# Optimization experiments

Hardware: AMD Instinct MI355X
Metric: run time of the kernel (lower is better)

The kernel has to match this reference:

```python
import jax, jax.numpy as jnp
import numpy as np

EMBED_CHOICES = (512, 768, 1024)
RATIO_CHOICES = (2, 3, 4)
D_MAX = 1024           # max embed_dim
H_MAX = 4096           # max expansion dim = 1024 * 4


def setup_inputs() -> dict:
    key = jax.random.key(0)
    ks = jax.random.split(key, 7)
    return {
        "x": jax.random.normal(ks[0], (8, 512, D_MAX), dtype=jnp.float32),
        "w0": jax.random.normal(ks[1], (H_MAX, D_MAX), dtype=jnp.float32) * 0.02,
        "b0": jax.random.normal(ks[2], (H_MAX,), dtype=jnp.float32) * 0.02,
        "w1": jax.random.normal(ks[3], (D_MAX, H_MAX), dtype=jnp.float32) * 0.02,
        "b1": jax.random.normal(ks[4], (D_MAX,), dtype=jnp.float32) * 0.02,
        "arch_embed": jax.random.normal(ks[5], (3,), dtype=jnp.float32),
        "arch_mlp": jax.random.normal(ks[6], (3,), dtype=jnp.float32),
    }


def _effective_masks(a, b):
    """Weighted-sum-of-sliced-linears == single linear with masked effective weights.

    Candidate (e, r): uses W0[:e*r, :e] on x[..., :e], zero-padded to H_MAX,
    and W1[:e, :e*r] on h[..., :e*r], zero-padded to D_MAX.
    """
    col = jnp.arange(D_MAX)
    row = jnp.arange(H_MAX)
    m0 = jnp.zeros((H_MAX, D_MAX), dtype=jnp.float32)
    bm0 = jnp.zeros((H_MAX,), dtype=jnp.float32)
    m1 = jnp.zeros((D_MAX, H_MAX), dtype=jnp.float32)
    bm1 = jnp.zeros((D_MAX,), dtype=jnp.float32)
    for ie, e in enumerate(EMBED_CHOICES):
        cm = (col < e).astype(jnp.float32)          # [D_MAX]
        for ir, r in enumerate(RATIO_CHOICES):
            w = a[ie] * b[ir]
            rm = (row < e * r).astype(jnp.float32)  # [H_MAX]
            m0 = m0 + w * rm[:, None] * cm[None, :]
            bm0 = bm0 + w * rm
            m1 = m1 + w * cm[:, None] * rm[None, :]
            bm1 = bm1 + w * cm
    return m0, bm0, m1, bm1


def reference(x, w0, b0, w1, b1, arch_embed, arch_mlp):
    a = jax.nn.softmax(arch_embed)  # DARTS-style arch weights over embed_dim
    b = jax.nn.softmax(arch_mlp)    # over mlp_ratio
    m0, bm0, m1, bm1 = _effective_masks(a, b)
    # layer 0 mix: [B,S,D] @ [D,H] -> [B,S,H]
    h = jnp.einsum("bsd,hd->bsh", x, m0 * w0) + bm0 * b0
    h = jax.nn.relu(h)
    # layer 1 mix: [B,S,H] @ [H,D] -> [B,S,D]
    out = jnp.einsum("bsh,dh->bsd", h, m1 * w1) + bm1 * b1
    # dropout p=0.0 (eval): identity
    return out
```

## Files before the change

### kernel.cpp

```cpp
#include <hip/hip_runtime.h>


typedef __attribute__((ext_vector_type(8))) short bf16x8;
typedef __attribute__((ext_vector_type(4))) float f32x4;
typedef __attribute__((ext_vector_type(8))) unsigned short u16x8;

__device__ __forceinline__ unsigned short f2bf(float f) {
  unsigned int x = __float_as_uint(f);
  x += 0x7fffu + ((x >> 16) & 1u);
  return (unsigned short)(x >> 16);
}

__device__ __forceinline__ void softmax3(const float* __restrict__ p, float* o) {
  float m = fmaxf(p[0], fmaxf(p[1], p[2]));
  float e0 = expf(p[0] - m), e1 = expf(p[1] - m), e2 = expf(p[2] - m);
  float inv = 1.0f / (e0 + e1 + e2);
  o[0] = e0 * inv; o[1] = e1 * inv; o[2] = e2 * inv;
}

__device__ __forceinline__ float sval(int h, int d, const float a[3], const float b[3]) {
  constexpr int E[3] = {512, 768, 1024};
  constexpr int R[3] = {2, 3, 4};
  float s = 0.f;
#pragma unroll
  for (int ie = 0; ie < 3; ++ie) {
    if (d < E[ie]) {
      float t = 0.f;
#pragma unroll
      for (int ir = 0; ir < 3; ++ir)
        if (h < E[ie] * R[ir]) t += b[ir];
      s += a[ie] * t;
    }
  }
  return s;
}


__global__ __launch_bounds__(256) void conv_x(const float* __restrict__ x,
                                              unsigned short* __restrict__ o,
                                              int n8) {
  int t = blockIdx.x * 256 + threadIdx.x;
  if (t >= n8) return;
  const f32x4* p = (const f32x4*)(x + (size_t)t * 8);
  f32x4 v0 = p[0], v1 = p[1];
  u16x8 r;
#pragma unroll
  for (int j = 0; j < 4; ++j) { r[j] = f2bf(v0[j]); r[4 + j] = f2bf(v1[j]); }
  *(u16x8*)(o + (size_t)t * 8) = r;
}

__global__ __launch_bounds__(256) void conv_w0(const float* __restrict__ w,
                                               const float* __restrict__ ae,
                                               const float* __restrict__ am,
                                               unsigned short* __restrict__ o) {
  int t = blockIdx.x * 256 + threadIdx.x;
  int base = t * 8;
  int h = base >> 10, d = base & 1023;
  float a[3], b[3];
  softmax3(ae, a); softmax3(am, b);
  float s = sval(h, d, a, b);
  const f32x4* p = (const f32x4*)(w + (size_t)base);
  f32x4 v0 = p[0], v1 = p[1];
  u16x8 r;
#pragma unroll
  for (int j = 0; j < 4; ++j) { r[j] = f2bf(v0[j] * s); r[4 + j] = f2bf(v1[j] * s); }
  *(u16x8*)(o + (size_t)base) = r;
}

__global__ __launch_bounds__(256) void conv_w1(const float* __restrict__ w,
                                               const float* __restrict__ ae,
                                               const float* __restrict__ am,
                                               unsigned short* __restrict__ o) {
  int t = blockIdx.x * 256 + threadIdx.x;
  int base = t * 8;
  int d = base >> 12, h = base & 4095;
  float a[3], b[3];
  softmax3(ae, a); softmax3(am, b);
  float s = sval(h, d, a, b);
  const f32x4* p = (const f32x4*)(w + (size_t)base);
  f32x4 v0 = p[0], v1 = p[1];
  u16x8 r;
#pragma unroll
  for (int j = 0; j < 4; ++j) { r[j] = f2bf(v0[j] * s); r[4 + j] = f2bf(v1[j] * s); }
  *(u16x8*)(o + (size_t)base) = r;
}

__global__ __launch_bounds__(256) void conv_bias(const float* __restrict__ b0,
                                                 const float* __restrict__ b1,
                                                 const float* __restrict__ ae,
                                                 const float* __restrict__ am,
                                                 float* __restrict__ bb0,
                                                 float* __restrict__ bb1) {
  int i = blockIdx.x * 256 + threadIdx.x;
  float a[3], b[3];
  softmax3(ae, a); softmax3(am, b);
  if (i < 4096) bb0[i] = sval(i, 0, a, b) * b0[i];
  int d = i - 4096;
  if (d >= 0 && d < 1024) bb1[d] = sval(0, d, a, b) * b1[d];
}


template <int MODE>
__device__ __forceinline__ void gemm_core(const unsigned short* __restrict__ A,
                                          const unsigned short* __restrict__ B,
                                          const float* __restrict__ bias,
                                          void* __restrict__ Cout,
                                          int M, int N, int K, int Ksub) {
  __shared__ unsigned short As[128 * 64];
  __shared__ unsigned short Bs[128 * 64];

  const int tid  = threadIdx.x;
  const int lane = tid & 63;
  const int w    = tid >> 6;
  const int m0   = blockIdx.x * 128;
  const int n0   = blockIdx.y * 128;
  const int wm   = (w >> 1) * 64;
  const int wn   = (w & 1) * 64;
  const int kbeg = (MODE == 2) ? blockIdx.z * Ksub : 0;
  const int kend = kbeg + Ksub;

  f32x4 acc[4][4] = {};

  const int srow = tid >> 3;
  const int scol = (tid & 7) * 8;
  const unsigned short* Ag = A + (size_t)(m0 + srow) * K + scol;
  const unsigned short* Bg = B + (size_t)(n0 + srow) * K + scol;
  unsigned short* Asl = As + tid * 8;
  unsigned short* Bsl = Bs + tid * 8;

  for (int k0 = kbeg; k0 < kend; k0 += 64) {
    __syncthreads();
#pragma unroll
    for (int i = 0; i < 4; ++i) {
      __builtin_amdgcn_global_load_lds(
          (const __attribute__((address_space(1))) void*)(Ag + (size_t)(i * 32) * K + k0),
          (__attribute__((address_space(3))) void*)(Asl + i * 2048), 16, 0, 0);
      __builtin_amdgcn_global_load_lds(
          (const __attribute__((address_space(1))) void*)(Bg + (size_t)(i * 32) * K + k0),
          (__attribute__((address_space(3))) void*)(Bsl + i * 2048), 16, 0, 0);
    }
    asm volatile("s_waitcnt vmcnt(0)" ::: "memory");
    __syncthreads();

#pragma unroll
    for (int ks = 0; ks < 2; ++ks) {
      const int ko = ks * 32 + (lane >> 4) * 8;
      bf16x8 af[4], bfr[4];
#pragma unroll
      for (int m = 0; m < 4; ++m)
        af[m] = *(const bf16x8*)&As[(wm + m * 16 + (lane & 15)) * 64 + ko];
#pragma unroll
      for (int n = 0; n < 4; ++n)
        bfr[n] = *(const bf16x8*)&Bs[(wn + n * 16 + (lane & 15)) * 64 + ko];
#pragma unroll
      for (int m = 0; m < 4; ++m)
#pragma unroll
        for (int n = 0; n < 4; ++n)
          acc[m][n] = __builtin_amdgcn_mfma_f32_16x16x32_bf16(af[m], bfr[n], acc[m][n], 0, 0, 0);
    }
  }

  const int crow = (lane >> 4) * 4;
  const int ccol = lane & 15;
#pragma unroll
  for (int m = 0; m < 4; ++m) {
#pragma unroll
    for (int n = 0; n < 4; ++n) {
      const int gr = m0 + wm + m * 16 + crow;
      const int gc = n0 + wn + n * 16 + ccol;
      if (MODE == 0) {
        const float bv = bias[gc];
        unsigned short* H = (unsigned short*)Cout;
#pragma unroll
        for (int r = 0; r < 4; ++r) {
          float v = fmaxf(acc[m][n][r] + bv, 0.f);
          H[(size_t)(gr + r) * N + gc] = f2bf(v);
        }
      } else if (MODE == 1) {
        const float bv = bias[gc];
        float* C = (float*)Cout;
#pragma unroll
        for (int r = 0; r < 4; ++r)
          C[(size_t)(gr + r) * N + gc] = acc[m][n][r] + bv;
      } else {
        float* P = (float*)Cout + (size_t)blockIdx.z * M * N;
#pragma unroll
        for (int r = 0; r < 4; ++r)
          P[(size_t)(gr + r) * N + gc] = acc[m][n][r];
      }
    }
  }
}

__global__ __launch_bounds__(256) void gemm_h(const unsigned short* __restrict__ A,
                                              const unsigned short* __restrict__ B,
                                              const float* __restrict__ bias,
                                              void* __restrict__ C,
                                              int M, int N, int K, int Ksub) {
  gemm_core<0>(A, B, bias, C, M, N, K, Ksub);
}
__global__ __launch_bounds__(256) void gemm_f(const unsigned short* __restrict__ A,
                                              const unsigned short* __restrict__ B,
                                              const float* __restrict__ bias,
                                              void* __restrict__ C,
                                              int M, int N, int K, int Ksub) {
  gemm_core<1>(A, B, bias, C, M, N, K, Ksub);
}
__global__ __launch_bounds__(256) void gemm_p(const unsigned short* __restrict__ A,
                                              const unsigned short* __restrict__ B,
                                              const float* __restrict__ bias,
                                              void* __restrict__ C,
                                              int M, int N, int K, int Ksub) {
  gemm_core<2>(A, B, bias, C, M, N, K, Ksub);
}

__global__ __launch_bounds__(256) void reduce_k(const float* __restrict__ P,
                                                const float* __restrict__ bb1,
                                                float* __restrict__ out,
                                                int n4) {
  const f32x4* p = (const f32x4*)P;
  const f32x4* bv = (const f32x4*)bb1;
  f32x4* o = (f32x4*)out;
  for (int i = blockIdx.x * 256 + threadIdx.x; i < n4; i += gridDim.x * 256) {
    f32x4 v = p[i];
    v += p[i + n4];
    v += p[i + 2 * n4];
    v += p[i + 3 * n4];
    v += bv[i & 255];
    o[i] = v;
  }
}


extern "C" void kernel_launch(void* const* d_in, const int* in_sizes, int n_in,
                              void* d_out, int out_size, void* d_ws, size_t ws_size,
                              hipStream_t stream) {
  const float* x  = (const float*)d_in[0];
  const float* w0 = (const float*)d_in[1];
  const float* b0 = (const float*)d_in[2];
  const float* w1 = (const float*)d_in[3];
  const float* b1 = (const float*)d_in[4];
  const float* ae = (const float*)d_in[5];
  const float* am = (const float*)d_in[6];

  char* ws = (char*)d_ws;
  unsigned short* xb   = (unsigned short*)(ws);
  unsigned short* w0e  = (unsigned short*)(ws + (8u  << 20));
  unsigned short* w1e  = (unsigned short*)(ws + (16u << 20));
  unsigned short* Hbuf = (unsigned short*)(ws + (24u << 20));
  float* bb0 = (float*)(ws + (56u << 20));
  float* bb1 = (float*)(ws + (56u << 20) + 16384);
  float* part = (float*)(ws + (57u << 20));
  const size_t WS_NEEDED = (57u << 20) + (64u << 20);

  conv_x  <<<2048, 256, 0, stream>>>(x, xb, 524288);
  conv_w0 <<<2048, 256, 0, stream>>>(w0, ae, am, w0e);
  conv_w1 <<<2048, 256, 0, stream>>>(w1, ae, am, w1e);
  conv_bias<<<20, 256, 0, stream>>>(b0, b1, ae, am, bb0, bb1);

  dim3 g1(32, 32);
  gemm_h<<<g1, 256, 0, stream>>>(xb, w0e, bb0, Hbuf, 4096, 4096, 1024, 1024);

  if (ws_size >= WS_NEEDED) {
    dim3 g2(32, 8, 4);
    gemm_p<<<g2, 256, 0, stream>>>(Hbuf, w1e, nullptr, part, 4096, 1024, 4096, 1024);
    reduce_k<<<2048, 256, 0, stream>>>(part, bb1, (float*)d_out, 1024 * 1024);
  } else {
    dim3 g2(32, 8);
    gemm_f<<<g2, 256, 0, stream>>>(Hbuf, w1e, bb1, d_out, 4096, 1024, 4096, 4096);
  }
}
```

Measured before the change: 223.6 us.

## Double-buffer GEMM LDS tiles and fuse conversion kernels into one launch

The GEMM main loop now uses two LDS buffers and issues global-to-LDS loads for the next K tile before computing the current one, waiting only on the older loads. This is meant to overlap memory latency with MFMA work. The four fp32-to-bf16 conversion and bias kernels are also merged into a single launch to cut launch overhead. Doubling LDS to 64KB per block may lower occupancy.

```diff
diff --git a/kernel.cpp b/kernel.cpp
--- a/kernel.cpp
+++ b/kernel.cpp
@@ -36,67 +36,49 @@
 }
 
 
-__global__ __launch_bounds__(256) void conv_x(const float* __restrict__ x,
-                                              unsigned short* __restrict__ o,
-                                              int n8) {
-  int t = blockIdx.x * 256 + threadIdx.x;
-  if (t >= n8) return;
-  const f32x4* p = (const f32x4*)(x + (size_t)t * 8);
+__device__ __forceinline__ void cvt8(const float* __restrict__ src,
+                                     unsigned short* __restrict__ dst,
+                                     size_t base, float s) {
+  const f32x4* p = (const f32x4*)(src + base);
   f32x4 v0 = p[0], v1 = p[1];
   u16x8 r;
 #pragma unroll
-  for (int j = 0; j < 4; ++j) { r[j] = f2bf(v0[j]); r[4 + j] = f2bf(v1[j]); }
-  *(u16x8*)(o + (size_t)t * 8) = r;
-}
-
-__global__ __launch_bounds__(256) void conv_w0(const float* __restrict__ w,
-                                               const float* __restrict__ ae,
-                                               const float* __restrict__ am,
-                                               unsigned short* __restrict__ o) {
+  for (int j = 0; j < 4; ++j) { r[j] = f2bf(v0[j] * s); r[4 + j] = f2bf(v1[j] * s); }
+  *(u16x8*)(dst + base) = r;
+}
+
+__global__ __launch_bounds__(256) void conv_all(const float* __restrict__ x,
+                                                const float* __restrict__ w0,
+                                                const float* __restrict__ b0,
+                                                const float* __restrict__ w1,
+                                                const float* __restrict__ b1,
+                                                const float* __restrict__ ae,
+                                                const float* __restrict__ am,
+                                                unsigned short* __restrict__ xb,
+                                                unsigned short* __restrict__ w0e,
+                                                unsigned short* __restrict__ w1e,
+                                                float* __restrict__ bb0,
+                                                float* __restrict__ bb1) {
   int t = blockIdx.x * 256 + threadIdx.x;
-  int base = t * 8;
-  int h = base >> 10, d = base & 1023;
   float a[3], b[3];
   softmax3(ae, a); softmax3(am, b);
-  float s = sval(h, d, a, b);
-  const f32x4* p = (const f32x4*)(w + (size_t)base);
-  f32x4 v0 = p[0], v1 = p[1];
-  u16x8 r;
-#pragma unroll
-  for (int j = 0; j < 4; ++j) { r[j] = f2bf(v0[j] * s); r[4 + j] = f2bf(v1[j] * s); }
-  *(u16x8*)(o + (size_t)base) = r;
-}
-
-__global__ __launch_bounds__(256) void conv_w1(const float* __restrict__ w,
-                                               const float* __restrict__ ae,
-                                               const float* __restrict__ am,
-                                               unsigned short* __restrict__ o) {
-  int t = blockIdx.x * 256 + threadIdx.x;
-  int base = t * 8;
-  int d = base >> 12, h = base & 4095;
-  float a[3], b[3];
-  softmax3(ae, a); softmax3(am, b);
-  float s = sval(h, d, a, b);
-  const f32x4* p = (const f32x4*)(w + (size_t)base);
-  f32x4 v0 = p[0], v1 = p[1];
-  u16x8 r;
-#pragma unroll
-  for (int j = 0; j < 4; ++j) { r[j] = f2bf(v0[j] * s); r[4 + j] = f2bf(v1[j] * s); }
-  *(u16x8*)(o + (size_t)base) = r;
-}
-
-__global__ __launch_bounds__(256) void conv_bias(const float* __restrict__ b0,
-                                                 const float* __restrict__ b1,
-                                                 const float* __restrict__ ae,
-                                                 const float* __restrict__ am,
-                                                 float* __restrict__ bb0,
-                                                 float* __restrict__ bb1) {
-  int i = blockIdx.x * 256 + threadIdx.x;
-  float a[3], b[3];
-  softmax3(ae, a); softmax3(am, b);
-  if (i < 4096) bb0[i] = sval(i, 0, a, b) * b0[i];
-  int d = i - 4096;
-  if (d >= 0 && d < 1024) bb1[d] = sval(0, d, a, b) * b1[d];
+  if (t < 524288) {
+    cvt8(x, xb, (size_t)t * 8, 1.0f);
+  } else if (t < 1048576) {
+    int base = (t - 524288) * 8;
+    cvt8(w0, w0e, base, sval(base >> 10, base & 1023, a, b));
+  } else if (t < 1572864) {
+    int base = (t - 1048576) * 8;
+    cvt8(w1, w1e, base, sval(base & 4095, base >> 12, a, b));
+  } else if (t < 1573504) {
+    int base = (t - 1572864) * 8;
+#pragma unroll
+    for (int j = 0; j < 8; ++j) {
+      int i = base + j;
+      if (i < 4096) bb0[i] = sval(i, 0, a, b) * b0[i];
+      else          bb1[i - 4096] = sval(0, i - 4096, a, b) * b1[i - 4096];
+    }
+  }
 }
 
 
@@ -106,8 +88,8 @@
                                           const float* __restrict__ bias,
                                           void* __restrict__ Cout,
                                           int M, int N, int K, int Ksub) {
-  __shared__ unsigned short As[128 * 64];
-  __shared__ unsigned short Bs[128 * 64];
+  __shared__ unsigned short As[2][128 * 64];
+  __shared__ unsigned short Bs[2][128 * 64];
 
   const int tid  = threadIdx.x;
   const int lane = tid & 63;
@@ -117,7 +99,7 @@
   const int wm   = (w >> 1) * 64;
   const int wn   = (w & 1) * 64;
   const int kbeg = (MODE == 2) ? blockIdx.z * Ksub : 0;
-  const int kend = kbeg + Ksub;
+  const int nt   = Ksub >> 6;
 
   f32x4 acc[4][4] = {};
 
@@ -125,22 +107,31 @@
   const int scol = (tid & 7) * 8;
   const unsigned short* Ag = A + (size_t)(m0 + srow) * K + scol;
   const unsigned short* Bg = B + (size_t)(n0 + srow) * K + scol;
-  unsigned short* Asl = As + tid * 8;
-  unsigned short* Bsl = Bs + tid * 8;
-
-  for (int k0 = kbeg; k0 < kend; k0 += 64) {
-    __syncthreads();
+
+  auto stage = [&](int buf, int k0) {
 #pragma unroll
     for (int i = 0; i < 4; ++i) {
       __builtin_amdgcn_global_load_lds(
           (const __attribute__((address_space(1))) void*)(Ag + (size_t)(i * 32) * K + k0),
-          (__attribute__((address_space(3))) void*)(Asl + i * 2048), 16, 0, 0);
+          (__attribute__((address_space(3))) void*)(&As[buf][0] + tid * 8 + i * 2048), 16, 0, 0);
       __builtin_amdgcn_global_load_lds(
           (const __attribute__((address_space(1))) void*)(Bg + (size_t)(i * 32) * K + k0),
-          (__attribute__((address_space(3))) void*)(Bsl + i * 2048), 16, 0, 0);
-    }
-    asm volatile("s_waitcnt vmcnt(0)" ::: "memory");
-    __syncthreads();
+          (__attribute__((address_space(3))) void*)(&Bs[buf][0] + tid * 8 + i * 2048), 16, 0, 0);
+    }
+  };
+
+  stage(0, kbeg);
+  int cur = 0;
+  for (int t = 0; t < nt; ++t) {
+    const int k0 = kbeg + t * 64;
+    if (t + 1 < nt) {
+      stage(cur ^ 1, k0 + 64);
+      asm volatile("s_waitcnt vmcnt(8)" ::: "memory");
+    } else {
+      asm volatile("s_waitcnt vmcnt(0)" ::: "memory");
+    }
+    __builtin_amdgcn_s_barrier();
+    asm volatile("" ::: "memory");
 
 #pragma unroll
     for (int ks = 0; ks < 2; ++ks) {
@@ -148,16 +139,20 @@
       bf16x8 af[4], bfr[4];
 #pragma unroll
       for (int m = 0; m < 4; ++m)
-        af[m] = *(const bf16x8*)&As[(wm + m * 16 + (lane & 15)) * 64 + ko];
+        af[m] = *(const bf16x8*)&As[cur][(wm + m * 16 + (lane & 15)) * 64 + ko];
 #pragma unroll
       for (int n = 0; n < 4; ++n)
-        bfr[n] = *(const bf16x8*)&Bs[(wn + n * 16 + (lane & 15)) * 64 + ko];
+        bfr[n] = *(const bf16x8*)&Bs[cur][(wn + n * 16 + (lane & 15)) * 64 + ko];
 #pragma unroll
       for (int m = 0; m < 4; ++m)
 #pragma unroll
         for (int n = 0; n < 4; ++n)
           acc[m][n] = __builtin_amdgcn_mfma_f32_16x16x32_bf16(af[m], bfr[n], acc[m][n], 0, 0, 0);
     }
+
+    asm volatile("s_waitcnt lgkmcnt(0)" ::: "memory");
+    __builtin_amdgcn_s_barrier();
+    cur ^= 1;
   }
 
   const int crow = (lane >> 4) * 4;
@@ -253,10 +248,8 @@
   float* part = (float*)(ws + (57u << 20));
   const size_t WS_NEEDED = (57u << 20) + (64u << 20);
 
-  conv_x  <<<2048, 256, 0, stream>>>(x, xb, 524288);
-  conv_w0 <<<2048, 256, 0, stream>>>(w0, ae, am, w0e);
-  conv_w1 <<<2048, 256, 0, stream>>>(w1, ae, am, w1e);
-  conv_bias<<<20, 256, 0, stream>>>(b0, b1, ae, am, bb0, bb1);
+  conv_all<<<6147, 256, 0, stream>>>(x, w0, b0, w1, b1, ae, am,
+                                     xb, w0e, w1e, bb0, bb1);
 
   dim3 g1(32, 32);
   gemm_h<<<g1, 256, 0, stream>>>(xb, w0e, bb0, Hbuf, 4096, 4096, 1024, 1024);
```

Measured after the change: 217.3 us. 2.8% less time.
